# Performance work log

Hardware: AMD Instinct MI355X
Metric: run time of the kernel (lower is better)

## Reference

```python
import jax, jax.numpy as jnp
import numpy as np

GAMMA = 1.4
CFL = 0.5
DX = 1e-3
ENTROPY_FIX = 0.1
NX = 1048576


def _roe_flux(rL, uL, pL, rR, uR, pR):
    """Roe flux with Harten entropy fix, vectorized over all interfaces."""
    g = GAMMA
    EL = pL / (g - 1) + 0.5 * rL * uL * uL
    ER = pR / (g - 1) + 0.5 * rR * uR * uR
    HL = (EL + pL) / rL
    HR = (ER + pR) / rR
    sL = jnp.sqrt(rL)
    sR = jnp.sqrt(rR)
    den = sL + sR
    ur = (sL * uL + sR * uR) / den
    Hr = (sL * HL + sR * HR) / den
    c = jnp.sqrt(jnp.clip((g - 1) * (Hr - 0.5 * ur * ur), 1e-10))
    eps = ENTROPY_FIX * c
    l1 = ur - c
    l3 = ur + c
    a1 = jnp.sqrt(l1 * l1 + eps * eps)
    a2 = jnp.sqrt(ur * ur + eps * eps)
    a3 = jnp.sqrt(l3 * l3 + eps * eps)
    drho = rR - rL
    du = uR - uL
    dp = pR - pL
    c2 = c * c
    al2 = drho - dp / c2
    al1 = (dp - c * rR * du) / (2 * c2)
    al3 = (dp + c * rR * du) / (2 * c2)
    FrL = rL * uL; FmL = rL * uL * uL + pL; FeL = uL * (EL + pL)
    FrR = rR * uR; FmR = rR * uR * uR + pR; FeR = uR * (ER + pR)
    dr = a1 * al1 + a2 * al2 + a3 * al3
    dm = a1 * al1 * l1 + a2 * al2 * ur + a3 * al3 * l3
    de = (a1 * al1 * (Hr - ur * c) + a2 * al2 * 0.5 * ur * ur
          + a3 * al3 * (Hr + ur * c))
    return (0.5 * (FrL + FrR - dr),
            0.5 * (FmL + FmR - dm),
            0.5 * (FeL + FeR - de))


def _step(carry, t_final):
    """One first-order Euler timestep with CFL-adaptive dt clipped to t_final."""
    rho, rhou, E, t = carry
    g = GAMMA
    u = rhou / rho
    p = (g - 1) * (E - 0.5 * rho * u * u)
    c = jnp.sqrt(g * p / rho)
    dt = CFL * DX / jnp.max(jnp.abs(u) + c)
    dt = jnp.minimum(dt, jnp.maximum(t_final - t, 0.0))
    # replicate edge ghost cells: [nx] -> [nx+2]
    rp = jnp.concatenate([rho[:1], rho, rho[-1:]])
    up = jnp.concatenate([u[:1], u, u[-1:]])
    pp = jnp.concatenate([p[:1], p, p[-1:]])
    # nx+1 interface fluxes
    Fr, Fm, Fe = _roe_flux(rp[:-1], up[:-1], pp[:-1], rp[1:], up[1:], pp[1:])
    dtdx = dt / DX
    return (rho - dtdx * (Fr[1:] - Fr[:-1]),
            rhou - dtdx * (Fm[1:] - Fm[:-1]),
            E - dtdx * (Fe[1:] - Fe[:-1]),
            t + dt)


def setup_inputs() -> dict:
    key = jax.random.key(0)
    k1, k2, k3 = jax.random.split(key, 3)
    rho = 1.0 + 0.5 * jax.random.uniform(k1, (NX,), jnp.float32)
    u = 0.1 * jax.random.normal(k2, (NX,), jnp.float32)
    p = 1.0 + 0.5 * jax.random.uniform(k3, (NX,), jnp.float32)
    return {"rho_init": rho, "u_init": u, "p_init": p,
            "t_final": jnp.float32(10.0), "n_steps": 32}


def reference(rho_init, u_init, p_init, t_final, n_steps):
    g = GAMMA
    rho = rho_init
    rhou = rho_init * u_init
    E = p_init / (g - 1) + 0.5 * rho_init * u_init ** 2
    body = jax.checkpoint(lambda c, _: (_step(c, t_final), None))
    (rho, rhou, E, _), _ = jax.lax.scan(
        body, (rho, rhou, E, jnp.float32(0.0)), None, length=n_steps)
    u = rhou / rho
    p = (g - 1) * (E - 0.5 * rho * u * u)
    return rho, u, p
```

## Files before the change

kernel.cpp:

```cpp
#include <hip/hip_runtime.h>


#define NXC   1048576
#define GAM   1.4f
#define GM1   0.4f
#define IGM1  2.5f
#define CFLC  0.5f
#define DXC   1e-3f
#define IDXC  1000.0f
#define EFIX  0.1f
#define NSTEPS 32
#define NSLOT  (NSTEPS + 1)

#define ABLK  1024
#define ACPT  4
#define ATILE (ABLK*ACPT)
#define ANBLK (NXC/ATILE)

#define CTRL_TOTAL (NSLOT * ANBLK)

__device__ __forceinline__ float frcp(float x){ return __builtin_amdgcn_rcpf(x); }
__device__ __forceinline__ float frsq(float x){ return __builtin_amdgcn_rsqf(x); }
__device__ __forceinline__ float fsqrt_(float x){ return __builtin_amdgcn_sqrtf(x); }

__device__ __forceinline__ float sysloadf(const float* p) {
    return __hip_atomic_load(p, __ATOMIC_RELAXED, __HIP_MEMORY_SCOPE_SYSTEM);
}
__device__ __forceinline__ void sysstoref(float* p, float v) {
    __hip_atomic_store(p, v, __ATOMIC_RELAXED, __HIP_MEMORY_SCOPE_SYSTEM);
}
__device__ __forceinline__ unsigned sysloadu(const unsigned* p) {
    return __hip_atomic_load(p, __ATOMIC_RELAXED, __HIP_MEMORY_SCOPE_SYSTEM);
}
__device__ __forceinline__ void sysstoreu(unsigned* p, unsigned v) {
    __hip_atomic_store(p, v, __ATOMIC_RELAXED, __HIP_MEMORY_SCOPE_SYSTEM);
}

__device__ __forceinline__ float wave_max(float v) {
    #pragma unroll
    for (int k = 32; k >= 1; k >>= 1)
        v = fmaxf(v, __shfl_xor(v, k));
    return v;
}

__global__ void bmax_init(unsigned* z) {
    int i = blockIdx.x * 256 + threadIdx.x;
    if (i < CTRL_TOTAL) z[i] = 0xAAAAAAAAu;
}

__device__ __forceinline__ void roe(
        float rL, float uL, float pL, float sL, float gL,
        float rR, float uR, float pR, float sR, float gR,
        float& Frj, float& Fmj, float& Fej) {
    float invden = frcp(sL + sR);
    float ur = (sL * uL + sR * uR) * invden;
    float Hr = (gL + gR) * invden;
    float c2u = fmaxf(GM1 * (Hr - 0.5f * ur * ur), 1e-10f);
    float qc = frsq(c2u);
    float c  = c2u * qc;
    float inv2c2 = 0.5f * qc * qc;
    float eps = EFIX * c;
    float l1 = ur - c, l3 = ur + c;
    float a1 = fsqrt_(l1 * l1 + eps * eps);
    float a2 = fsqrt_(ur * ur + eps * eps);
    float a3 = fsqrt_(l3 * l3 + eps * eps);
    float drho = rR - rL;
    float du   = uR - uL;
    float dp   = pR - pL;
    float al2 = drho - (dp + dp) * inv2c2;
    float tcd = c * rR * du;
    float al1 = (dp - tcd) * inv2c2;
    float al3 = (dp + tcd) * inv2c2;
    float FrL = rL * uL, FrR = rR * uR;
    float FmL = FrL * uL + pL, FmR = FrR * uR + pR;
    float FeL = uL * (gL * sL), FeR = uR * (gR * sR);
    float w1 = a1 * al1, w2 = a2 * al2, w3 = a3 * al3;
    Frj = 0.5f * (FrL + FrR - (w1 + w2 + w3));
    Fmj = 0.5f * (FmL + FmR - (w1 * l1 + w2 * ur + w3 * l3));
    Fej = 0.5f * (FeL + FeR - (w1 * (Hr - ur * c) + w2 * (0.5f * ur * ur)
                               + w3 * (Hr + ur * c)));
}

__global__ __launch_bounds__(ABLK, 4) void euler_async(
        const float* __restrict__ rho0, const float* __restrict__ u0,
        const float* __restrict__ p0, const float* __restrict__ tf,
        float* __restrict__ out, unsigned* __restrict__ bmax,
        float* __restrict__ halo) {
    __shared__ float Lr[ABLK], Lu[ABLK], Lp[ABLK];
    __shared__ float fxr[ABLK], fxm[ABLK], fxe[ABLK];
    __shared__ float red[ABLK / 64];
    __shared__ float samax;

    const int tid = threadIdx.x, bid = blockIdx.x;
    const int c0 = bid * ATILE + ACPT * tid;
    const int lane = tid & 63, wid = tid >> 6;

    float cr[4], cu[4], cp[4], cE[4], cs[4], cg[4];

    {
        float4 r4 = *(const float4*)(rho0 + c0);
        float4 u4 = *(const float4*)(u0 + c0);
        float4 p4 = *(const float4*)(p0 + c0);
        cr[0]=r4.x; cr[1]=r4.y; cr[2]=r4.z; cr[3]=r4.w;
        cu[0]=u4.x; cu[1]=u4.y; cu[2]=u4.z; cu[3]=u4.w;
        cp[0]=p4.x; cp[1]=p4.y; cp[2]=p4.z; cp[3]=p4.w;
        float nm = 0.f;
        #pragma unroll
        for (int c = 0; c < 4; ++c) {
            float E = cp[c] * IGM1 + 0.5f * cr[c] * cu[c] * cu[c];
            float q = frsq(cr[c]);
            cE[c] = E;
            cs[c] = cr[c] * q;
            cg[c] = (E + cp[c]) * q;
            nm = fmaxf(nm, fabsf(cu[c]) + fsqrt_(GAM * cp[c] * (q * q)));
        }
        Lr[tid]=cr[3]; Lu[tid]=cu[3]; Lp[tid]=cp[3];
        if (tid == 0) {
            float* h = halo + (size_t)bid * 6;
            sysstoref(h, cr[0]); sysstoref(h+1, cu[0]); sysstoref(h+2, cp[0]);
        }
        if (tid == ABLK - 1) {
            float* h = halo + (size_t)bid * 6 + 3;
            sysstoref(h, cr[3]); sysstoref(h+1, cu[3]); sysstoref(h+2, cp[3]);
        }
        nm = wave_max(nm);
        if (lane == 0) red[wid] = nm;
        __syncthreads();
        if (tid < ABLK / 64) {
            float bm = red[tid];
            bm = fmaxf(bm, __shfl_xor(bm, 8));
            bm = fmaxf(bm, __shfl_xor(bm, 4));
            bm = fmaxf(bm, __shfl_xor(bm, 2));
            bm = fmaxf(bm, __shfl_xor(bm, 1));
            if (tid == 0) sysstoreu(&bmax[bid], __float_as_uint(bm));
        }
    }
    float t = 0.f;
    const float tfin = *tf;

    for (int k = 0; k < NSTEPS; ++k) {
        const unsigned* brow = bmax + (size_t)k * ANBLK;
        float Fr[5], Fm[5], Fe[5];

        float rl, ul, pl;
        float r5 = 0.f, u5 = 0.f, p5 = 0.f;
        if (tid == 0) {
            if (bid > 0) {
                while (sysloadu(&brow[bid - 1]) & 0x80000000u)
                    __builtin_amdgcn_s_sleep(1);
                const float* h = halo + ((size_t)k * ANBLK + (bid - 1)) * 6 + 3;
                rl = sysloadf(h); ul = sysloadf(h+1); pl = sysloadf(h+2);
            } else { rl = cr[0]; ul = cu[0]; pl = cp[0]; }
        } else { rl = Lr[tid-1]; ul = Lu[tid-1]; pl = Lp[tid-1]; }
        if (tid == ABLK - 1) {
            if (bid < ANBLK - 1) {
                while (sysloadu(&brow[bid + 1]) & 0x80000000u)
                    __builtin_amdgcn_s_sleep(1);
                const float* h = halo + ((size_t)k * ANBLK + (bid + 1)) * 6;
                r5 = sysloadf(h); u5 = sysloadf(h+1); p5 = sysloadf(h+2);
            } else { r5 = cr[3]; u5 = cu[3]; p5 = cp[3]; }
        }

        roe(cr[0],cu[0],cp[0],cs[0],cg[0], cr[1],cu[1],cp[1],cs[1],cg[1],
            Fr[1], Fm[1], Fe[1]);
        roe(cr[1],cu[1],cp[1],cs[1],cg[1], cr[2],cu[2],cp[2],cs[2],cg[2],
            Fr[2], Fm[2], Fe[2]);
        roe(cr[2],cu[2],cp[2],cs[2],cg[2], cr[3],cu[3],cp[3],cs[3],cg[3],
            Fr[3], Fm[3], Fe[3]);

        {
            float El = pl * IGM1 + 0.5f * rl * ul * ul;
            float ql = frsq(rl);
            float sl = rl * ql, gl = (El + pl) * ql;
            roe(rl,ul,pl,sl,gl, cr[0],cu[0],cp[0],cs[0],cg[0],
                Fr[0], Fm[0], Fe[0]);
            fxr[tid] = Fr[0]; fxm[tid] = Fm[0]; fxe[tid] = Fe[0];
        }

        if (tid == ABLK - 1) {
            float E5 = p5 * IGM1 + 0.5f * r5 * u5 * u5;
            float q5 = frsq(r5);
            float s5 = r5 * q5, g5 = (E5 + p5) * q5;
            roe(cr[3],cu[3],cp[3],cs[3],cg[3], r5,u5,p5,s5,g5,
                Fr[4], Fm[4], Fe[4]);
        }

        if (wid == 0) {
            unsigned v0, v1, v2, v3;
            for (;;) {
                v0 = sysloadu(&brow[lane]);
                v1 = sysloadu(&brow[64 + lane]);
                v2 = sysloadu(&brow[128 + lane]);
                v3 = sysloadu(&brow[192 + lane]);
                if (__all(((v0 | v1 | v2 | v3) & 0x80000000u) == 0u)) break;
                __builtin_amdgcn_s_sleep(1);
            }
            float m = fmaxf(fmaxf(__uint_as_float(v0), __uint_as_float(v1)),
                            fmaxf(__uint_as_float(v2), __uint_as_float(v3)));
            m = wave_max(m);
            if (lane == 0) samax = m;
        }

        __syncthreads();

        if (tid < ABLK - 1) {
            Fr[4] = fxr[tid + 1]; Fm[4] = fxm[tid + 1]; Fe[4] = fxe[tid + 1];
        }
        float amax = samax;
        float dt = fminf((CFLC * DXC) * frcp(amax), fmaxf(tfin - t, 0.f));
        t += dt;
        float dtdx = dt * IDXC;

        float nm = 0.f;
        #pragma unroll
        for (int c = 0; c < 4; ++c) {
            float r2 = cr[c]         - dtdx * (Fr[c+1] - Fr[c]);
            float m2 = cr[c] * cu[c] - dtdx * (Fm[c+1] - Fm[c]);
            float E2 = cE[c]         - dtdx * (Fe[c+1] - Fe[c]);
            float q2 = frsq(r2);
            float ir = q2 * q2;
            float u2 = m2 * ir;
            float p2 = GM1 * (E2 - 0.5f * r2 * u2 * u2);
            cr[c]=r2; cu[c]=u2; cp[c]=p2; cE[c]=E2;
            cs[c]=r2 * q2;
            cg[c]=(E2 + p2) * q2;
            nm = fmaxf(nm, fabsf(u2) + fsqrt_(GAM * p2 * ir));
        }

        if (k < NSTEPS - 1) {
            Lr[tid]=cr[3]; Lu[tid]=cu[3]; Lp[tid]=cp[3];
            if (tid == 0) {
                float* h = halo + ((size_t)(k + 1) * ANBLK + bid) * 6;
                sysstoref(h, cr[0]); sysstoref(h+1, cu[0]); sysstoref(h+2, cp[0]);
            }
            if (tid == ABLK - 1) {
                float* h = halo + ((size_t)(k + 1) * ANBLK + bid) * 6 + 3;
                sysstoref(h, cr[3]); sysstoref(h+1, cu[3]); sysstoref(h+2, cp[3]);
            }
            nm = wave_max(nm);
            if (lane == 0) red[wid] = nm;
            __syncthreads();
            if (tid < ABLK / 64) {
                float bm = red[tid];
                bm = fmaxf(bm, __shfl_xor(bm, 8));
                bm = fmaxf(bm, __shfl_xor(bm, 4));
                bm = fmaxf(bm, __shfl_xor(bm, 2));
                bm = fmaxf(bm, __shfl_xor(bm, 1));
                if (tid == 0)
                    sysstoreu(&bmax[(size_t)(k + 1) * ANBLK + bid],
                              __float_as_uint(bm));
            }
        } else {
            *(float4*)(out + c0)         = make_float4(cr[0], cr[1], cr[2], cr[3]);
            *(float4*)(out + NXC + c0)   = make_float4(cu[0], cu[1], cu[2], cu[3]);
            *(float4*)(out + 2*NXC + c0) = make_float4(cp[0], cp[1], cp[2], cp[3]);
        }
    }
}

extern "C" void kernel_launch(void* const* d_in, const int* in_sizes, int n_in,
                              void* d_out, int out_size, void* d_ws, size_t ws_size,
                              hipStream_t stream) {
    const float* rho0 = (const float*)d_in[0];
    const float* u0   = (const float*)d_in[1];
    const float* p0   = (const float*)d_in[2];
    const float* tf   = (const float*)d_in[3];

    float* out      = (float*)d_out;
    unsigned* bmax  = (unsigned*)d_ws;
    float* halo     = (float*)(bmax + CTRL_TOTAL);

    bmax_init<<<(CTRL_TOTAL + 255) / 256, 256, 0, stream>>>(bmax);

    void* args[] = {(void*)&rho0, (void*)&u0, (void*)&p0, (void*)&tf,
                    (void*)&out, (void*)&bmax, (void*)&halo};
    hipLaunchCooperativeKernel((void*)euler_async, dim3(ANBLK), dim3(ABLK),
                               args, 0, stream);
}
```

Before: 211.0 us.

## Use agent-scope atomics and remap blocks so halo neighbours share an XCD

Inter-block halo and max-wavespeed exchanges now use agent (device) scope atomics instead of system scope. This is meant to avoid system-coherent cache bypass on the polling and publish path. Logical block indices are also remapped so that consecutive blocks dispatched round-robin across the 8 XCDs get contiguous tiles. Most halo neighbours should then sit on the same die, which should cut cross-die L2 traffic. The risk is that agent-scope visibility across XCDs depends on cache coherence behaviour, and the mapping assumes round-robin dispatch.

```diff
diff --git a/kernel.cpp b/kernel.cpp
--- a/kernel.cpp
+++ b/kernel.cpp
@@ -23,17 +23,17 @@
 __device__ __forceinline__ float frsq(float x){ return __builtin_amdgcn_rsqf(x); }
 __device__ __forceinline__ float fsqrt_(float x){ return __builtin_amdgcn_sqrtf(x); }
 
-__device__ __forceinline__ float sysloadf(const float* p) {
-    return __hip_atomic_load(p, __ATOMIC_RELAXED, __HIP_MEMORY_SCOPE_SYSTEM);
-}
-__device__ __forceinline__ void sysstoref(float* p, float v) {
-    __hip_atomic_store(p, v, __ATOMIC_RELAXED, __HIP_MEMORY_SCOPE_SYSTEM);
-}
-__device__ __forceinline__ unsigned sysloadu(const unsigned* p) {
-    return __hip_atomic_load(p, __ATOMIC_RELAXED, __HIP_MEMORY_SCOPE_SYSTEM);
-}
-__device__ __forceinline__ void sysstoreu(unsigned* p, unsigned v) {
-    __hip_atomic_store(p, v, __ATOMIC_RELAXED, __HIP_MEMORY_SCOPE_SYSTEM);
+__device__ __forceinline__ float devloadf(const float* p) {
+    return __hip_atomic_load(p, __ATOMIC_RELAXED, __HIP_MEMORY_SCOPE_AGENT);
+}
+__device__ __forceinline__ void devstoref(float* p, float v) {
+    __hip_atomic_store(p, v, __ATOMIC_RELAXED, __HIP_MEMORY_SCOPE_AGENT);
+}
+__device__ __forceinline__ unsigned devloadu(const unsigned* p) {
+    return __hip_atomic_load(p, __ATOMIC_RELAXED, __HIP_MEMORY_SCOPE_AGENT);
+}
+__device__ __forceinline__ void devstoreu(unsigned* p, unsigned v) {
+    __hip_atomic_store(p, v, __ATOMIC_RELAXED, __HIP_MEMORY_SCOPE_AGENT);
 }
 
 __device__ __forceinline__ float wave_max(float v) {
@@ -91,8 +91,9 @@
     __shared__ float red[ABLK / 64];
     __shared__ float samax;
 
-    const int tid = threadIdx.x, bid = blockIdx.x;
-    const int c0 = bid * ATILE + ACPT * tid;
+    const int tid = threadIdx.x;
+    const int lb = (blockIdx.x & 7) * (ANBLK / 8) + (blockIdx.x >> 3);
+    const int c0 = lb * ATILE + ACPT * tid;
     const int lane = tid & 63, wid = tid >> 6;
 
     float cr[4], cu[4], cp[4], cE[4], cs[4], cg[4];
@@ -116,12 +117,12 @@
         }
         Lr[tid]=cr[3]; Lu[tid]=cu[3]; Lp[tid]=cp[3];
         if (tid == 0) {
-            float* h = halo + (size_t)bid * 6;
-            sysstoref(h, cr[0]); sysstoref(h+1, cu[0]); sysstoref(h+2, cp[0]);
+            float* h = halo + (size_t)lb * 6;
+            devstoref(h, cr[0]); devstoref(h+1, cu[0]); devstoref(h+2, cp[0]);
         }
         if (tid == ABLK - 1) {
-            float* h = halo + (size_t)bid * 6 + 3;
-            sysstoref(h, cr[3]); sysstoref(h+1, cu[3]); sysstoref(h+2, cp[3]);
+            float* h = halo + (size_t)lb * 6 + 3;
+            devstoref(h, cr[3]); devstoref(h+1, cu[3]); devstoref(h+2, cp[3]);
         }
         nm = wave_max(nm);
         if (lane == 0) red[wid] = nm;
@@ -132,7 +133,7 @@
             bm = fmaxf(bm, __shfl_xor(bm, 4));
             bm = fmaxf(bm, __shfl_xor(bm, 2));
             bm = fmaxf(bm, __shfl_xor(bm, 1));
-            if (tid == 0) sysstoreu(&bmax[bid], __float_as_uint(bm));
+            if (tid == 0) devstoreu(&bmax[lb], __float_as_uint(bm));
         }
     }
     float t = 0.f;
@@ -145,19 +146,19 @@
         float rl, ul, pl;
         float r5 = 0.f, u5 = 0.f, p5 = 0.f;
         if (tid == 0) {
-            if (bid > 0) {
-                while (sysloadu(&brow[bid - 1]) & 0x80000000u)
+            if (lb > 0) {
+                while (devloadu(&brow[lb - 1]) & 0x80000000u)
                     __builtin_amdgcn_s_sleep(1);
-                const float* h = halo + ((size_t)k * ANBLK + (bid - 1)) * 6 + 3;
-                rl = sysloadf(h); ul = sysloadf(h+1); pl = sysloadf(h+2);
+                const float* h = halo + ((size_t)k * ANBLK + (lb - 1)) * 6 + 3;
+                rl = devloadf(h); ul = devloadf(h+1); pl = devloadf(h+2);
             } else { rl = cr[0]; ul = cu[0]; pl = cp[0]; }
         } else { rl = Lr[tid-1]; ul = Lu[tid-1]; pl = Lp[tid-1]; }
         if (tid == ABLK - 1) {
-            if (bid < ANBLK - 1) {
-                while (sysloadu(&brow[bid + 1]) & 0x80000000u)
+            if (lb < ANBLK - 1) {
+                while (devloadu(&brow[lb + 1]) & 0x80000000u)
                     __builtin_amdgcn_s_sleep(1);
-                const float* h = halo + ((size_t)k * ANBLK + (bid + 1)) * 6;
-                r5 = sysloadf(h); u5 = sysloadf(h+1); p5 = sysloadf(h+2);
+                const float* h = halo + ((size_t)k * ANBLK + (lb + 1)) * 6;
+                r5 = devloadf(h); u5 = devloadf(h+1); p5 = devloadf(h+2);
             } else { r5 = cr[3]; u5 = cu[3]; p5 = cp[3]; }
         }
 
@@ -188,10 +189,10 @@
         if (wid == 0) {
             unsigned v0, v1, v2, v3;
             for (;;) {
-                v0 = sysloadu(&brow[lane]);
-                v1 = sysloadu(&brow[64 + lane]);
-                v2 = sysloadu(&brow[128 + lane]);
-                v3 = sysloadu(&brow[192 + lane]);
+                v0 = devloadu(&brow[lane]);
+                v1 = devloadu(&brow[64 + lane]);
+                v2 = devloadu(&brow[128 + lane]);
+                v3 = devloadu(&brow[192 + lane]);
                 if (__all(((v0 | v1 | v2 | v3) & 0x80000000u) == 0u)) break;
                 __builtin_amdgcn_s_sleep(1);
             }
@@ -230,12 +231,12 @@
         if (k < NSTEPS - 1) {
             Lr[tid]=cr[3]; Lu[tid]=cu[3]; Lp[tid]=cp[3];
             if (tid == 0) {
-                float* h = halo + ((size_t)(k + 1) * ANBLK + bid) * 6;
-                sysstoref(h, cr[0]); sysstoref(h+1, cu[0]); sysstoref(h+2, cp[0]);
+                float* h = halo + ((size_t)(k + 1) * ANBLK + lb) * 6;
+                devstoref(h, cr[0]); devstoref(h+1, cu[0]); devstoref(h+2, cp[0]);
             }
             if (tid == ABLK - 1) {
-                float* h = halo + ((size_t)(k + 1) * ANBLK + bid) * 6 + 3;
-                sysstoref(h, cr[3]); sysstoref(h+1, cu[3]); sysstoref(h+2, cp[3]);
+                float* h = halo + ((size_t)(k + 1) * ANBLK + lb) * 6 + 3;
+                devstoref(h, cr[3]); devstoref(h+1, cu[3]); devstoref(h+2, cp[3]);
             }
             nm = wave_max(nm);
             if (lane == 0) red[wid] = nm;
@@ -247,7 +248,7 @@
                 bm = fmaxf(bm, __shfl_xor(bm, 2));
                 bm = fmaxf(bm, __shfl_xor(bm, 1));
                 if (tid == 0)
-                    sysstoreu(&bmax[(size_t)(k + 1) * ANBLK + bid],
+                    devstoreu(&bmax[(size_t)(k + 1) * ANBLK + lb],
                               __float_as_uint(bm));
             }
         } else {
```

Result: faster. 203.7 us (-3.5%).
